# Kernel tuning notes

Measured on AMD Instinct MI355X. Metric: run time of the kernel, lower is better.

## Reference

```python
import jax, jax.numpy as jnp
import numpy as np

B, T, N, K, HD = 4, 32, 1024, 16, 128
IN_CH = 4


def _knn_idx(q, r, k):
    # q, r: [..., 3, N]. dist(n, m) = ||q[..., n] - r[..., m]||
    # expanded-norm form avoids materializing [..., 3, N, N]
    q2 = jnp.sum(q * q, axis=-2)                     # [..., N]
    r2 = jnp.sum(r * r, axis=-2)                     # [..., N]
    qr = jnp.einsum('...cn,...cm->...nm', q, r)      # [..., N, N]
    d2 = q2[..., :, None] + r2[..., None, :] - 2.0 * qr
    _, idx = jax.lax.top_k(-d2, k)                   # smallest-k (sqrt is monotone)
    return idx                                       # [..., N, K]


def _gather_nbrs(feat, idx):
    # feat [B, C, N], idx [B, N, K] -> [B, C, N, K]; out[b,c,n,k] = feat[b,c,idx[b,n,k]]
    return jax.vmap(lambda f, i: f[:, i])(feat, idx)


def _lstm_layer(cur_in, position, pos_past, group_ind, w, b, hd):
    # cur_in [B,T,C,N]; position/pos_past [B,T,4,N]; group_ind [B,T,N,K]
    Bb, Tt, C, Nn = cur_in.shape
    h0 = jnp.zeros((Bb, hd, Nn), cur_in.dtype)
    c0 = jnp.zeros_like(h0)

    def step(carry, inp):
        h, c = carry                                  # [B,hd,N]
        xt, pp, idx = inp                             # [B,C,N], [B,4,N], [B,N,K]
        h_with_pos = jnp.concatenate([pp, h], axis=1) # [B,4+hd,N]
        hg = _gather_nbrs(h_with_pos, idx)            # [B,4+hd,N,K]
        cg = _gather_nbrs(c, idx)                     # [B,hd,N,K]
        # cell subtracts center position from first 4 channels of hidden
        hg = jnp.concatenate([hg[:, :4] - xt[:, :4, :, None], hg[:, 4:]], axis=1)
        xk = jnp.broadcast_to(xt[..., None], xt.shape + (idx.shape[-1],))
        comb = jnp.concatenate([xk, hg], axis=1)      # [B, C+4+hd, N, K]
        gates = jnp.einsum('bink,oi->bonk', comb, w) + b[None, :, None, None]
        ci, cf, co, cgt = jnp.split(gates, 4, axis=1)
        c_next = jax.nn.sigmoid(cf) * cg + jax.nn.sigmoid(ci) * jnp.tanh(cgt)
        h_next = jax.nn.sigmoid(co) * jnp.tanh(c_next)
        h_new = jnp.max(h_next, axis=-1)              # AdaptiveMaxPool2d((None,1)) over K
        c_new = jnp.max(c_next, axis=-1)
        return (h_new, c_new), h_new

    xs = (jnp.moveaxis(cur_in, 1, 0), jnp.moveaxis(pos_past, 1, 0),
          jnp.moveaxis(group_ind, 1, 0))
    (h, c), hs = jax.lax.scan(step, (h0, c0), xs)
    hs = jnp.moveaxis(hs, 0, 1)                       # [B,T,hd,N]
    layer_out = jnp.concatenate([position, hs], axis=2)  # [B,T,4+hd,N]
    return layer_out, h, c


def _forward(x, w0, b0, w1, b1):
    position = x[:, :, :4]                            # [B,T,4,N]
    p3 = position[:, :, :3]
    idx0 = _knn_idx(p3[:, 0], p3[:, 0], K)[:, None]   # [B,1,N,K] (frame 0 vs itself)
    idxr = _knn_idx(p3[:, 1:], p3[:, :-1], K)         # [B,T-1,N,K] (frame t vs t-1)
    group_ind = jnp.concatenate([idx0, idxr], axis=1)  # [B,T,N,K]
    # past-frame positions (t=0 uses frame 0)
    pos_past = jnp.concatenate([position[:, :1], position[:, :-1]], axis=1)
    out0, h, c = _lstm_layer(x,    position, pos_past, group_ind, w0, b0, HD)
    out1, h, c = _lstm_layer(out0, position, pos_past, group_ind, w1, b1, HD)
    return out1, h, c, group_ind


def setup_inputs() -> dict:
    key = jax.random.key(0)
    ks = jax.random.split(key, 3)
    x = jax.random.normal(ks[0], (B, T, IN_CH, N), jnp.float32)
    # 1x1 conv weights flattened to [out, in]; layer0 in=4+4+128=136, layer1 in=132+4+128=264
    w0 = jax.random.normal(ks[1], (4 * HD, IN_CH + 4 + HD), jnp.float32) * 0.05
    b0 = jnp.zeros((4 * HD,), jnp.float32)
    w1 = jax.random.normal(ks[2], (4 * HD, (HD + 4) + 4 + HD), jnp.float32) * 0.05
    b1 = jnp.zeros((4 * HD,), jnp.float32)
    return {"x": x, "w0": w0, "b0": b0, "w1": w1, "b1": b1}


def reference(x, w0, b0, w1, b1):
    out1, h, c, group_ind = _forward(x, w0, b0, w1, b1)
    # match torch shapes: trailing singleton dim
    return out1[..., None], h[..., None], c[..., None], group_ind
```

## Files before the change

### kernel.cpp

```cpp
#include <hip/hip_runtime.h>
#include <math.h>

#define BB 4
#define TT 32
#define NN 1024
#define KK 16
#define HDIM 128
#define NO 512
#define KG 132

#define OUT1_SZ ((size_t)BB*TT*132*NN)
#define OH (OUT1_SZ)
#define OC (OH + (size_t)BB*HDIM*NN)
#define OG (OC + (size_t)BB*HDIM*NN)

__global__ __launch_bounds__(256) void prep_weights(
    const float* __restrict__ w0, const float* __restrict__ w1,
    float* __restrict__ WaT0, float* __restrict__ WgT0,
    float* __restrict__ WaT1, float* __restrict__ WgT1)
{
  int idx = blockIdx.x * 256 + threadIdx.x;
  if (idx >= KG * NO) return;
  int k = idx / NO, o = idx - k * NO;
  WgT0[idx] = w0[o * 136 + 4 + k];
  WgT1[idx] = w1[o * 264 + 132 + k];
  float a1 = w1[o * 264 + k];
  if (k < 4) a1 -= w1[o * 264 + 132 + k];
  WaT1[idx] = a1;
  if (k < 4) WaT0[k * NO + o] = w0[o * 136 + k] - w0[o * 136 + 4 + k];
}

__global__ __launch_bounds__(512) void knn_kernel(
    const float* __restrict__ x, int* __restrict__ gind, float* __restrict__ gfloat)
{
  __shared__ float rx[NN], ry[NN], rz[NN], rr[NN];
  int b = blockIdx.z, t = blockIdx.y;
  int tp = (t == 0) ? 0 : t - 1;
  const float* xr = x + (size_t)(b * TT + tp) * 4 * NN;
  for (int m = threadIdx.x; m < NN; m += 512) {
    float a = xr[m], e = xr[NN + m], c = xr[2 * NN + m];
    rx[m] = a; ry[m] = e; rz[m] = c;
    rr[m] = __fadd_rn(__fadd_rn(__fmul_rn(a, a), __fmul_rn(e, e)), __fmul_rn(c, c));
  }
  __syncthreads();
  int n = blockIdx.x * 512 + threadIdx.x;
  const float* xq = x + (size_t)(b * TT + t) * 4 * NN;
  float qx = xq[n], qy = xq[NN + n], qz = xq[2 * NN + n];
  float q2 = __fadd_rn(__fadd_rn(__fmul_rn(qx, qx), __fmul_rn(qy, qy)), __fmul_rn(qz, qz));
  float bd[KK]; int bi[KK];
#pragma unroll
  for (int i = 0; i < KK; ++i) { bd[i] = 3.402823466e38f; bi[i] = 0; }
  for (int m = 0; m < NN; ++m) {
    float s = __fmaf_rn(qz, rz[m], __fmaf_rn(qy, ry[m], __fmaf_rn(qx, rx[m], 0.0f)));
    float d2 = __fsub_rn(__fadd_rn(q2, rr[m]), __fmul_rn(2.0f, s));
    if (d2 < bd[KK - 1]) {
#pragma unroll
      for (int i = KK - 1; i > 0; --i) {
        float pv = bd[i - 1]; int pi = bi[i - 1];
        if (pv > d2)            { bd[i] = pv; bi[i] = pi; }
        else if (bd[i] > d2)    { bd[i] = d2; bi[i] = m; }
      }
      if (bd[0] > d2) { bd[0] = d2; bi[0] = m; }
    }
  }
  size_t base = ((size_t)(b * TT + t) * NN + n) * KK;
#pragma unroll
  for (int i = 0; i < KK; ++i) { gind[base + i] = bi[i]; gfloat[base + i] = (float)bi[i]; }
}

template<int KA>
__global__ __launch_bounds__(256) void gemm_ag(
    const float* __restrict__ WgT, const float* __restrict__ WaT,
    const float* __restrict__ bias, const float* __restrict__ x,
    const float* __restrict__ hTg, size_t hTg_bstr,
    const float* __restrict__ hTa,
    int t, int tp,
    float* __restrict__ Aout, float* __restrict__ Gout)
{
  int tid = threadIdx.x;
  int w = tid >> 6, lane = tid & 63;
  int bid = blockIdx.x;
  int b = (bid >> 1) & 3;
  int sub = (bid >> 3) * 2 + (bid & 1);
  int ob = sub >> 4, nb = sub & 15;
  int o0u = __builtin_amdgcn_readfirstlane(ob * 16 + w * 4);
  int n = nb * 64 + lane;

  float aG[4] = {0.f, 0.f, 0.f, 0.f};
  float aA[4] = {0.f, 0.f, 0.f, 0.f};

  const float* xg = x + (size_t)(b * TT + tp) * 4 * NN + n;
  const float* xa = x + (size_t)(b * TT + t) * 4 * NN + n;

#pragma unroll
  for (int k = 0; k < 4; ++k) {
    const float* wg = WgT + (size_t)k * NO + o0u;
    const float* wa = WaT + (size_t)k * NO + o0u;
    float gv = xg[(size_t)k * NN];
    float av = xa[(size_t)k * NN];
#pragma unroll
    for (int i = 0; i < 4; ++i) {
      aG[i] = fmaf(wg[i], gv, aG[i]);
      aA[i] = fmaf(wa[i], av, aA[i]);
    }
  }

  const float* hg = hTg + (size_t)b * hTg_bstr + n;
  const float* ha = hTa + (size_t)b * (HDIM * NN) + n;
#pragma unroll 4
  for (int k = 0; k < HDIM; ++k) {
    const float* wg = WgT + (size_t)(4 + k) * NO + o0u;
    float gv = hg[(size_t)k * NN];
#pragma unroll
    for (int i = 0; i < 4; ++i) aG[i] = fmaf(wg[i], gv, aG[i]);
    if (KA == 132) {
      const float* wa = WaT + (size_t)(4 + k) * NO + o0u;
      float av = ha[(size_t)k * NN];
#pragma unroll
      for (int i = 0; i < 4; ++i) aA[i] = fmaf(wa[i], av, aA[i]);
    }
  }

  const float* bv = bias + o0u;
  size_t row = ((size_t)b * NN + n) * NO + o0u;
  *(float4*)&Gout[row] = make_float4(aG[0], aG[1], aG[2], aG[3]);
  *(float4*)&Aout[row] = make_float4(aA[0] + bv[0], aA[1] + bv[1],
                                     aA[2] + bv[2], aA[3] + bv[3]);
}

__global__ __launch_bounds__(1024) void ew_step(
    const float* __restrict__ A, const float* __restrict__ G,
    const int* __restrict__ gind,
    const float* __restrict__ c_in, float* __restrict__ c_out,
    float* __restrict__ hT, size_t hT_bstr, int t)
{
  __shared__ float htile[HDIM][9];
  int tid = threadIdx.x;
  int j = tid & 127, ns = tid >> 7;
  int bid = blockIdx.x;
  int b = (bid >> 1) & 3;
  int nb8 = (bid >> 3) * 2 + (bid & 1);
  int n = nb8 * 8 + ns;
  const float* Ap = A + ((size_t)b * NN + n) * NO;
  float a0 = Ap[j], a1 = Ap[128 + j], a2 = Ap[256 + j], a3 = Ap[384 + j];
  const int* ip = gind + ((size_t)(b * TT + t) * NN + n) * KK;
  const float* Gb = G + (size_t)b * NN * NO;
  const float* cb = c_in + (size_t)b * NN * HDIM;
  float hmax = -3.402823466e38f, cmax = -3.402823466e38f;
#pragma unroll 4
  for (int k = 0; k < KK; ++k) {
    int m = __builtin_amdgcn_readfirstlane(ip[k]);
    const float* Gp = Gb + (size_t)m * NO;
    float gi = a0 + Gp[j];
    float gf = a1 + Gp[128 + j];
    float go = a2 + Gp[256 + j];
    float gg = a3 + Gp[384 + j];
    float cg = cb[(size_t)m * HDIM + j];
    float si = 1.0f / (1.0f + __expf(-gi));
    float sf = 1.0f / (1.0f + __expf(-gf));
    float so = 1.0f / (1.0f + __expf(-go));
    float tg = 1.0f - 2.0f / (1.0f + __expf(2.0f * gg));
    float cn = sf * cg + si * tg;
    float tc = 1.0f - 2.0f / (1.0f + __expf(2.0f * cn));
    float hn = so * tc;
    hmax = fmaxf(hmax, hn);
    cmax = fmaxf(cmax, cn);
  }
  c_out[((size_t)b * NN + n) * HDIM + j] = cmax;
  htile[j][ns] = hmax;
  __syncthreads();
  int jw = tid >> 3, nn = tid & 7;
  hT[(size_t)b * hT_bstr + (size_t)jw * NN + nb8 * 8 + nn] = htile[jw][nn];
}

__global__ __launch_bounds__(256) void transpose_nj_jn(
    const float* __restrict__ src, float* __restrict__ dst,
    size_t dstBase, size_t bStride)
{
  __shared__ float tl[64][65];
  int tid = threadIdx.x;
  int n0 = blockIdx.x * 64, j0 = blockIdx.y * 64, b = blockIdx.z;
  int c = tid & 63, r4 = tid >> 6;
#pragma unroll
  for (int i = 0; i < 16; ++i) {
    int r = r4 + i * 4;
    tl[r][c] = src[((size_t)b * NN + n0 + r) * HDIM + j0 + c];
  }
  __syncthreads();
  float* dp = dst + dstBase + (size_t)b * bStride;
#pragma unroll
  for (int i = 0; i < 16; ++i) {
    int rr = r4 + i * 4;
    dp[(size_t)(j0 + rr) * NN + n0 + c] = tl[c][rr];
  }
}

__global__ __launch_bounds__(256) void copy_h(const float* __restrict__ out1,
                                              float* __restrict__ dst)
{
  int i = blockIdx.x * 256 + threadIdx.x;
  if (i >= BB * HDIM * NN) return;
  int b = i / (HDIM * NN);
  int r = i - b * (HDIM * NN);
  dst[i] = out1[((size_t)(b * TT + TT - 1) * 132 + 4) * NN + r];
}

__global__ __launch_bounds__(256) void pos_copy(const float* __restrict__ x,
                                                float* __restrict__ out)
{
  int i = blockIdx.x * 256 + threadIdx.x;
  if (i >= BB * TT * 4 * NN) return;
  int n = i & (NN - 1);
  int btc = i >> 10;
  int c = btc & 3, bt = btc >> 2;
  out[((size_t)bt * 132 + c) * NN + n] = x[i];
}

extern "C" void kernel_launch(void* const* d_in, const int* in_sizes, int n_in,
                              void* d_out, int out_size, void* d_ws, size_t ws_size,
                              hipStream_t stream)
{
  const float* x  = (const float*)d_in[0];
  const float* w0 = (const float*)d_in[1];
  const float* b0 = (const float*)d_in[2];
  const float* w1 = (const float*)d_in[3];
  const float* b1 = (const float*)d_in[4];
  float* out = (float*)d_out;

  float* wsf = (float*)d_ws;
  int*   gind = (int*)d_ws;
  size_t off = (size_t)BB * TT * NN * KK;
  const size_t HSZ = (size_t)BB * NN * HDIM;
  float* h0T = wsf + off; off += HSZ;
  float* c0a = wsf + off; off += HSZ;
  float* c0b = wsf + off; off += HSZ;
  float* c1a = wsf + off; off += HSZ;
  float* c1b = wsf + off; off += HSZ;
  float* zeros = wsf + off; off += (size_t)HDIM * NN;
  float* Abuf = wsf + off; off += (size_t)BB * NN * NO;
  float* Gbuf = wsf + off; off += (size_t)BB * NN * NO;
  float* WaT0 = wsf + off; off += 4 * NO;
  float* WgT0 = wsf + off; off += (size_t)KG * NO;
  float* WaT1 = wsf + off; off += (size_t)KG * NO;
  float* WgT1 = wsf + off; off += (size_t)KG * NO;

  hipMemsetAsync(c0a, 0, HSZ * 4, stream);
  hipMemsetAsync(c1a, 0, HSZ * 4, stream);
  hipMemsetAsync(zeros, 0, (size_t)HDIM * NN * 4, stream);

  prep_weights<<<(KG * NO + 255) / 256, 256, 0, stream>>>(w0, w1, WaT0, WgT0, WaT1, WgT1);
  knn_kernel<<<dim3(2, TT, BB), 512, 0, stream>>>(x, gind, out + OG);
  pos_copy<<<(BB * TT * 4 * NN + 255) / 256, 256, 0, stream>>>(x, out);

  const size_t H_BSTR = (size_t)HDIM * NN;
  const size_t OUT_BSTR = (size_t)TT * 132 * NN;

  float* c0[2] = {c0a, c0b};
  float* c1[2] = {c1a, c1b};
  for (int t = 0; t < TT; ++t) {
    int tp = t ? t - 1 : 0;
    const float* hTg0 = t ? h0T : zeros;
    gemm_ag<4><<<dim3(2048), 256, 0, stream>>>(
        WgT0, WaT0, b0, x, hTg0, t ? H_BSTR : 0, h0T, t, tp, Abuf, Gbuf);
    ew_step<<<dim3(512), 1024, 0, stream>>>(
        Abuf, Gbuf, gind, c0[t & 1], c0[(t & 1) ^ 1], h0T, H_BSTR, t);
    const float* hTg1 = t ? (out + ((size_t)(t - 1) * 132 + 4) * NN) : zeros;
    gemm_ag<132><<<dim3(2048), 256, 0, stream>>>(
        WgT1, WaT1, b1, x, hTg1, t ? OUT_BSTR : 0, h0T, t, tp, Abuf, Gbuf);
    ew_step<<<dim3(512), 1024, 0, stream>>>(
        Abuf, Gbuf, gind, c1[t & 1], c1[(t & 1) ^ 1],
        out + ((size_t)t * 132 + 4) * NN, OUT_BSTR, t);
  }
  copy_h<<<(BB * HDIM * NN + 255) / 256, 256, 0, stream>>>(out, out + OH);
  transpose_nj_jn<<<dim3(16, 2, BB), 256, 0, stream>>>(c1[0], out, OC, (size_t)HDIM * NN);
}
```

Baseline: 3.845 ms.

## Wavefront-pipeline the two LSTM layers, fusing layer1 step t with layer0 step t+1

The two stacked LSTM layers now run as a skewed wavefront. Layer 1 at step t and layer 0 at step t+1 are computed together in one fused GEMM kernel (gemm3) and one fused elementwise kernel (ew2), with the roles split across blocks. This roughly halves the number of dependent kernel launches and raises per-launch parallelism for the small recurrent steps. It also shares the h0 loads between the layer-0 G and layer-1 A GEMMs. In exchange it doubles the A/G workspace buffers and gives each fused GEMM thread more accumulators, which raises register pressure.

```diff
diff --git a/kernel.cpp b/kernel.cpp
--- a/kernel.cpp
+++ b/kernel.cpp
@@ -13,6 +13,9 @@
 #define OH (OUT1_SZ)
 #define OC (OH + (size_t)BB*HDIM*NN)
 #define OG (OC + (size_t)BB*HDIM*NN)
+
+#define H_BSTR ((size_t)HDIM * NN)
+#define OUT_BSTR ((size_t)TT * 132 * NN)
 
 __global__ __launch_bounds__(256) void prep_weights(
     const float* __restrict__ w0, const float* __restrict__ w1,
@@ -106,7 +109,7 @@
   }
 
   const float* hg = hTg + (size_t)b * hTg_bstr + n;
-  const float* ha = hTa + (size_t)b * (HDIM * NN) + n;
+  const float* ha = hTa + (size_t)b * H_BSTR + n;
 #pragma unroll 4
   for (int k = 0; k < HDIM; ++k) {
     const float* wg = WgT + (size_t)(4 + k) * NO + o0u;
@@ -128,19 +131,90 @@
                                      aA[2] + bv[2], aA[3] + bv[3]);
 }
 
-__global__ __launch_bounds__(1024) void ew_step(
+__global__ __launch_bounds__(256) void gemm3(
+    const float* __restrict__ WgT0, const float* __restrict__ WgT1,
+    const float* __restrict__ WaT1, const float* __restrict__ WaT0,
+    const float* __restrict__ b1v, const float* __restrict__ b0v,
+    const float* __restrict__ x,
+    const float* __restrict__ h1src, size_t h1bstr,
+    const float* __restrict__ h0T,
+    int tg, int t0, int ta0,
+    float* __restrict__ G1out, float* __restrict__ A1out,
+    float* __restrict__ G0out, float* __restrict__ A0out)
+{
+  int tid = threadIdx.x;
+  int w = tid >> 6, lane = tid & 63;
+  int bid = blockIdx.x;
+  int b = (bid >> 1) & 3;
+  int sub = (bid >> 3) * 2 + (bid & 1);
+  int ob = sub >> 4, nb = sub & 15;
+  int o0u = __builtin_amdgcn_readfirstlane(ob * 16 + w * 4);
+  int n = nb * 64 + lane;
+
+  float aG1[4] = {0.f, 0.f, 0.f, 0.f};
+  float aA1[4] = {0.f, 0.f, 0.f, 0.f};
+  float aG0[4] = {0.f, 0.f, 0.f, 0.f};
+  float aA0[4] = {0.f, 0.f, 0.f, 0.f};
+
+  const float* xg = x + (size_t)(b * TT + tg) * 4 * NN + n;
+  const float* xa = x + (size_t)(b * TT + t0) * 4 * NN + n;
+  const float* x0 = x + (size_t)(b * TT + ta0) * 4 * NN + n;
+
+#pragma unroll
+  for (int k = 0; k < 4; ++k) {
+    const float* wg1 = WgT1 + (size_t)k * NO + o0u;
+    const float* wa1 = WaT1 + (size_t)k * NO + o0u;
+    const float* wg0 = WgT0 + (size_t)k * NO + o0u;
+    const float* wa0 = WaT0 + (size_t)k * NO + o0u;
+    float gv = xg[(size_t)k * NN];
+    float av = xa[(size_t)k * NN];
+    float a0v = x0[(size_t)k * NN];
+#pragma unroll
+    for (int i = 0; i < 4; ++i) {
+      aG1[i] = fmaf(wg1[i], gv, aG1[i]);
+      aA1[i] = fmaf(wa1[i], av, aA1[i]);
+      aG0[i] = fmaf(wg0[i], av, aG0[i]);
+      aA0[i] = fmaf(wa0[i], a0v, aA0[i]);
+    }
+  }
+
+  const float* h1 = h1src + (size_t)b * h1bstr + n;
+  const float* h0 = h0T + (size_t)b * H_BSTR + n;
+#pragma unroll 4
+  for (int k = 0; k < HDIM; ++k) {
+    const float* wg1 = WgT1 + (size_t)(4 + k) * NO + o0u;
+    const float* wa1 = WaT1 + (size_t)(4 + k) * NO + o0u;
+    const float* wg0 = WgT0 + (size_t)(4 + k) * NO + o0u;
+    float g1v = h1[(size_t)k * NN];
+    float h0v = h0[(size_t)k * NN];
+#pragma unroll
+    for (int i = 0; i < 4; ++i) {
+      aG1[i] = fmaf(wg1[i], g1v, aG1[i]);
+      aA1[i] = fmaf(wa1[i], h0v, aA1[i]);
+      aG0[i] = fmaf(wg0[i], h0v, aG0[i]);
+    }
+  }
+
+  const float* bv1 = b1v + o0u;
+  const float* bv0 = b0v + o0u;
+  size_t row = ((size_t)b * NN + n) * NO + o0u;
+  *(float4*)&G1out[row] = make_float4(aG1[0], aG1[1], aG1[2], aG1[3]);
+  *(float4*)&A1out[row] = make_float4(aA1[0] + bv1[0], aA1[1] + bv1[1],
+                                      aA1[2] + bv1[2], aA1[3] + bv1[3]);
+  *(float4*)&G0out[row] = make_float4(aG0[0], aG0[1], aG0[2], aG0[3]);
+  *(float4*)&A0out[row] = make_float4(aA0[0] + bv0[0], aA0[1] + bv0[1],
+                                      aA0[2] + bv0[2], aA0[3] + bv0[3]);
+}
+
+__device__ __forceinline__ void ew_body(
+    int b, int n, int nb8, int tid, int t,
     const float* __restrict__ A, const float* __restrict__ G,
     const int* __restrict__ gind,
     const float* __restrict__ c_in, float* __restrict__ c_out,
-    float* __restrict__ hT, size_t hT_bstr, int t)
-{
-  __shared__ float htile[HDIM][9];
-  int tid = threadIdx.x;
+    float* __restrict__ hT, size_t hT_bstr,
+    float (*htile)[9])
+{
   int j = tid & 127, ns = tid >> 7;
-  int bid = blockIdx.x;
-  int b = (bid >> 1) & 3;
-  int nb8 = (bid >> 3) * 2 + (bid & 1);
-  int n = nb8 * 8 + ns;
   const float* Ap = A + ((size_t)b * NN + n) * NO;
   float a0 = Ap[j], a1 = Ap[128 + j], a2 = Ap[256 + j], a3 = Ap[384 + j];
   const int* ip = gind + ((size_t)(b * TT + t) * NN + n) * KK;
@@ -173,6 +247,50 @@
   hT[(size_t)b * hT_bstr + (size_t)jw * NN + nb8 * 8 + nn] = htile[jw][nn];
 }
 
+__global__ __launch_bounds__(1024) void ew_step(
+    const float* __restrict__ A, const float* __restrict__ G,
+    const int* __restrict__ gind,
+    const float* __restrict__ c_in, float* __restrict__ c_out,
+    float* __restrict__ hT, size_t hT_bstr, int t)
+{
+  __shared__ float htile[HDIM][9];
+  int bid = blockIdx.x;
+  int b = (bid >> 1) & 3;
+  int nb8 = (bid >> 3) * 2 + (bid & 1);
+  int tid = threadIdx.x;
+  int n = nb8 * 8 + (tid >> 7);
+  ew_body(b, n, nb8, tid, t, A, G, gind, c_in, c_out, hT, hT_bstr, htile);
+}
+
+__global__ __launch_bounds__(1024) void ew2(
+    const float* __restrict__ A1, const float* __restrict__ G1,
+    const float* __restrict__ A0, const float* __restrict__ G0,
+    const int* __restrict__ gind,
+    const float* __restrict__ c1in, float* __restrict__ c1out,
+    const float* __restrict__ c0in, float* __restrict__ c0out,
+    float* __restrict__ h1out, float* __restrict__ h0T,
+    int t1, int t0)
+{
+  __shared__ float htile[HDIM][9];
+  int bid = blockIdx.x;
+  int role = bid & 1;
+  int sub = bid >> 1;
+  int b = (sub >> 1) & 3;
+  int nb8 = (sub >> 3) * 2 + (sub & 1);
+  int tid = threadIdx.x;
+  int n = nb8 * 8 + (tid >> 7);
+
+  const float* A   = role ? A1 : A0;
+  const float* G   = role ? G1 : G0;
+  const float* cin = role ? c1in : c0in;
+  float* cout      = role ? c1out : c0out;
+  float* hT        = role ? h1out : h0T;
+  size_t hbstr     = role ? OUT_BSTR : H_BSTR;
+  int t            = role ? t1 : t0;
+
+  ew_body(b, n, nb8, tid, t, A, G, gind, cin, cout, hT, hbstr, htile);
+}
+
 __global__ __launch_bounds__(256) void transpose_nj_jn(
     const float* __restrict__ src, float* __restrict__ dst,
     size_t dstBase, size_t bStride)
@@ -237,8 +355,10 @@
   float* c1a = wsf + off; off += HSZ;
   float* c1b = wsf + off; off += HSZ;
   float* zeros = wsf + off; off += (size_t)HDIM * NN;
-  float* Abuf = wsf + off; off += (size_t)BB * NN * NO;
-  float* Gbuf = wsf + off; off += (size_t)BB * NN * NO;
+  float* A1buf = wsf + off; off += (size_t)BB * NN * NO;
+  float* G1buf = wsf + off; off += (size_t)BB * NN * NO;
+  float* A0buf = wsf + off; off += (size_t)BB * NN * NO;
+  float* G0buf = wsf + off; off += (size_t)BB * NN * NO;
   float* WaT0 = wsf + off; off += 4 * NO;
   float* WgT0 = wsf + off; off += (size_t)KG * NO;
   float* WaT1 = wsf + off; off += (size_t)KG * NO;
@@ -252,25 +372,37 @@
   knn_kernel<<<dim3(2, TT, BB), 512, 0, stream>>>(x, gind, out + OG);
   pos_copy<<<(BB * TT * 4 * NN + 255) / 256, 256, 0, stream>>>(x, out);
 
-  const size_t H_BSTR = (size_t)HDIM * NN;
-  const size_t OUT_BSTR = (size_t)TT * 132 * NN;
-
   float* c0[2] = {c0a, c0b};
   float* c1[2] = {c1a, c1b};
-  for (int t = 0; t < TT; ++t) {
-    int tp = t ? t - 1 : 0;
-    const float* hTg0 = t ? h0T : zeros;
-    gemm_ag<4><<<dim3(2048), 256, 0, stream>>>(
-        WgT0, WaT0, b0, x, hTg0, t ? H_BSTR : 0, h0T, t, tp, Abuf, Gbuf);
-    ew_step<<<dim3(512), 1024, 0, stream>>>(
-        Abuf, Gbuf, gind, c0[t & 1], c0[(t & 1) ^ 1], h0T, H_BSTR, t);
-    const float* hTg1 = t ? (out + ((size_t)(t - 1) * 132 + 4) * NN) : zeros;
-    gemm_ag<132><<<dim3(2048), 256, 0, stream>>>(
-        WgT1, WaT1, b1, x, hTg1, t ? OUT_BSTR : 0, h0T, t, tp, Abuf, Gbuf);
-    ew_step<<<dim3(512), 1024, 0, stream>>>(
-        Abuf, Gbuf, gind, c1[t & 1], c1[(t & 1) ^ 1],
-        out + ((size_t)t * 132 + 4) * NN, OUT_BSTR, t);
-  }
+
+  gemm_ag<4><<<dim3(2048), 256, 0, stream>>>(
+      WgT0, WaT0, b0, x, zeros, 0, h0T, 0, 0, A0buf, G0buf);
+  ew_step<<<dim3(512), 1024, 0, stream>>>(
+      A0buf, G0buf, gind, c0a, c0b, h0T, H_BSTR, 0);
+  gemm3<<<dim3(2048), 256, 0, stream>>>(
+      WgT0, WgT1, WaT1, WaT0, b1, b0, x,
+      zeros, 0, h0T, 0, 0, 1,
+      G1buf, A1buf, G0buf, A0buf);
+
+  for (int t1 = 0; t1 < TT - 1; ++t1) {
+    int t0 = t1 + 1;
+    ew2<<<dim3(1024), 1024, 0, stream>>>(
+        A1buf, G1buf, A0buf, G0buf, gind,
+        c1[t1 & 1], c1[(t1 & 1) ^ 1],
+        c0[t0 & 1], c0[(t0 & 1) ^ 1],
+        out + ((size_t)t1 * 132 + 4) * NN, h0T, t1, t0);
+    int ta0 = (t0 + 1 < TT) ? t0 + 1 : TT - 1;
+    gemm3<<<dim3(2048), 256, 0, stream>>>(
+        WgT0, WgT1, WaT1, WaT0, b1, b0, x,
+        out + ((size_t)t1 * 132 + 4) * NN, OUT_BSTR, h0T,
+        t1, t0, ta0,
+        G1buf, A1buf, G0buf, A0buf);
+  }
+
+  ew_step<<<dim3(512), 1024, 0, stream>>>(
+      A1buf, G1buf, gind, c1b, c1a,
+      out + ((size_t)(TT - 1) * 132 + 4) * NN, OUT_BSTR, TT - 1);
+
   copy_h<<<(BB * HDIM * NN + 255) / 256, 256, 0, stream>>>(out, out + OH);
-  transpose_nj_jn<<<dim3(16, 2, BB), 256, 0, stream>>>(c1[0], out, OC, (size_t)HDIM * NN);
-}
+  transpose_nj_jn<<<dim3(16, 2, BB), 256, 0, stream>>>(c1a, out, OC, (size_t)HDIM * NN);
+}
```

New measurement: 3.741 ms. 1.03x faster.
